# Kernel tuning notes

Hardware: AMD Instinct MI355X
Metric: run time of the kernel (lower is better)

## Reference

```python
import jax, jax.numpy as jnp
import numpy as np

H = 512

def _lstm_dir(seq, Wih, Whh, bih, bhh, reverse):
    # seq: [B,S,in]; Wih: [4H,in]; Whh: [4H,H]; biases [4H]
    B = seq.shape[0]
    xp = jnp.einsum('bsi,gi->bsg', seq, Wih) + bih  # precompute input projection [B,S,4H]
    h0 = jnp.zeros((B, H), seq.dtype)
    c0 = jnp.zeros((B, H), seq.dtype)

    def step(carry, xt):
        h, c = carry
        g = xt + h @ Whh.T + bhh
        i, f, gg, o = jnp.split(g, 4, axis=-1)
        c = jax.nn.sigmoid(f) * c + jax.nn.sigmoid(i) * jnp.tanh(gg)
        h = jax.nn.sigmoid(o) * jnp.tanh(c)
        return (h, c), h

    _, hs = jax.lax.scan(step, (h0, c0), jnp.swapaxes(xp, 0, 1), reverse=reverse)
    return jnp.swapaxes(hs, 0, 1)  # [B,S,H]


def setup_inputs() -> dict:
    key = jax.random.key(0)
    ks = jax.random.split(key, 24)
    B, S, E, V, C = 32, 512, 512, 32000, 2
    sc = 0.1
    d = {
        'x': jax.random.randint(ks[0], (B, S), 0, V, dtype=jnp.int32),
        'attention_mask': jnp.ones((B, S), dtype=jnp.int32),
        'emb': jax.random.normal(ks[1], (V, E), jnp.float32) * sc,
        'fc_W': jax.random.normal(ks[2], (C, 2 * H), jnp.float32) * sc,
        'fc_b': jax.random.normal(ks[3], (C,), jnp.float32) * sc,
    }
    i = 4
    for l, insz in [(0, E), (1, 2 * H)]:
        for dname in ('fwd', 'bwd'):
            d[f'{dname}_Wih{l}'] = jax.random.normal(ks[i], (4 * H, insz), jnp.float32) * sc; i += 1
            d[f'{dname}_Whh{l}'] = jax.random.normal(ks[i], (4 * H, H), jnp.float32) * sc; i += 1
            d[f'{dname}_bih{l}'] = jax.random.normal(ks[i], (4 * H,), jnp.float32) * sc; i += 1
            d[f'{dname}_bhh{l}'] = jax.random.normal(ks[i], (4 * H,), jnp.float32) * sc; i += 1
    return d


def reference(x, attention_mask, emb, fc_W, fc_b,
              fwd_Wih0, fwd_Whh0, fwd_bih0, fwd_bhh0,
              bwd_Wih0, bwd_Whh0, bwd_bih0, bwd_bhh0,
              fwd_Wih1, fwd_Whh1, fwd_bih1, fwd_bhh1,
              bwd_Wih1, bwd_Whh1, bwd_bih1, bwd_bhh1):
    out = emb[x]  # [B,S,E]
    layers = [
        ((fwd_Wih0, fwd_Whh0, fwd_bih0, fwd_bhh0), (bwd_Wih0, bwd_Whh0, bwd_bih0, bwd_bhh0)),
        ((fwd_Wih1, fwd_Whh1, fwd_bih1, fwd_bhh1), (bwd_Wih1, bwd_Whh1, bwd_bih1, bwd_bhh1)),
    ]
    for fw, bw in layers:
        f = _lstm_dir(out, *fw, reverse=False)
        b = _lstm_dir(out, *bw, reverse=True)
        out = jnp.concatenate([f, b], axis=-1)  # [B,S,2H]
        # dropout is identity in eval mode
    mask = attention_mask.astype(out.dtype)
    pooled = (out * mask[..., None]).sum(axis=1) / jnp.clip(mask.sum(axis=1, keepdims=True), 1e-9)
    logits = pooled @ fc_W.T + fc_b
    return logits
```

## Files before the change

kernel.cpp:

```cpp
#include <hip/hip_runtime.h>

typedef unsigned short u16;
typedef unsigned int   u32;
typedef unsigned long long u64;
typedef __attribute__((ext_vector_type(8))) short bf16x8;
typedef __attribute__((ext_vector_type(4))) float f32x4;

__device__ __forceinline__ u16 f2bf(float f) {
    u32 u; __builtin_memcpy(&u, &f, 4);
    u32 r = (u + 0x7FFFu + ((u >> 16) & 1u)) >> 16;
    return (u16)r;
}
__device__ __forceinline__ float bf2f(u16 h) {
    u32 u = ((u32)h) << 16; float f; __builtin_memcpy(&f, &u, 4); return f;
}
__device__ __forceinline__ float sigmoidf(float x) { return 1.f / (1.f + __expf(-x)); }
__device__ __forceinline__ float tanh_safe(float x) {
    float e = __expf(-2.f * fabsf(x));
    float t = (1.f - e) / (1.f + e);
    return x >= 0.f ? t : -t;
}

__global__ __launch_bounds__(256) void castk2(const float* __restrict__ s, u16* __restrict__ hi,
                                              u16* __restrict__ lo, int n) {
    int i = blockIdx.x * 256 + threadIdx.x;
    if (i < n) {
        float f = s[i];
        u16 h = f2bf(f);
        hi[i] = h;
        lo[i] = f2bf(f - bf2f(h));
    }
}

__global__ __launch_bounds__(256) void embed_cast(const int* __restrict__ x, const float* __restrict__ emb,
                                                  u16* __restrict__ x0) {
    int m = blockIdx.x;
    int idx = x[m];
    const float2* src = (const float2*)(emb + (size_t)idx * 512);
    u16* dst = x0 + (size_t)m * 512;
    int t = threadIdx.x;
    float2 v = src[t];
    dst[t * 2]     = f2bf(v.x);
    dst[t * 2 + 1] = f2bf(v.y);
}

__global__ __launch_bounds__(256) void gemm_bt(const u16* __restrict__ A, const u16* __restrict__ Bhi,
                                               const u16* __restrict__ Blo,
                                               u16* __restrict__ C, int M, int N, int K) {
    __shared__ __align__(16) u16 sA[128 * 32];
    __shared__ __align__(16) u16 sBh[128 * 32];
    __shared__ __align__(16) u16 sBl[128 * 32];
    const int tid  = threadIdx.x;
    const int lane = tid & 63, wave = tid >> 6;
    const int m0 = blockIdx.y * 128, n0 = blockIdx.x * 128;
    const int wm = (wave >> 1) * 64, wn = (wave & 1) * 64;
    f32x4 acc[4][4] = {};

    const int r0 = tid >> 2, c8 = (tid & 3) * 8;
    const int r1 = r0 + 64;
    const u16* Ap   = A   + (size_t)(m0 + r0) * K + c8;
    const u16* Ap2  = A   + (size_t)(m0 + r1) * K + c8;
    const u16* Bhp  = Bhi + (size_t)(n0 + r0) * K + c8;
    const u16* Bhp2 = Bhi + (size_t)(n0 + r1) * K + c8;
    const u16* Blp  = Blo + (size_t)(n0 + r0) * K + c8;
    const u16* Blp2 = Blo + (size_t)(n0 + r1) * K + c8;

    uint4 ra0, ra1, rh0, rh1, rl0, rl1;
    ra0 = *(const uint4*)(Ap);   ra1 = *(const uint4*)(Ap2);
    rh0 = *(const uint4*)(Bhp);  rh1 = *(const uint4*)(Bhp2);
    rl0 = *(const uint4*)(Blp);  rl1 = *(const uint4*)(Blp2);

    for (int kk = 0; kk < K; kk += 32) {
        __syncthreads();
        *(uint4*)(sA  + tid * 8)        = ra0;
        *(uint4*)(sA  + 2048 + tid * 8) = ra1;
        *(uint4*)(sBh + tid * 8)        = rh0;
        *(uint4*)(sBh + 2048 + tid * 8) = rh1;
        *(uint4*)(sBl + tid * 8)        = rl0;
        *(uint4*)(sBl + 2048 + tid * 8) = rl1;
        int kn = kk + 32;
        if (kn < K) {
            ra0 = *(const uint4*)(Ap + kn);   ra1 = *(const uint4*)(Ap2 + kn);
            rh0 = *(const uint4*)(Bhp + kn);  rh1 = *(const uint4*)(Bhp2 + kn);
            rl0 = *(const uint4*)(Blp + kn);  rl1 = *(const uint4*)(Blp2 + kn);
        }
        __syncthreads();
        bf16x8 av[4], bh[4], bl[4];
#pragma unroll
        for (int i = 0; i < 4; ++i) {
            av[i] = *(const bf16x8*)(sA  + (wm + i * 16 + (lane & 15)) * 32 + (lane >> 4) * 8);
            bh[i] = *(const bf16x8*)(sBh + (wn + i * 16 + (lane & 15)) * 32 + (lane >> 4) * 8);
            bl[i] = *(const bf16x8*)(sBl + (wn + i * 16 + (lane & 15)) * 32 + (lane >> 4) * 8);
        }
#pragma unroll
        for (int i = 0; i < 4; ++i)
#pragma unroll
            for (int j = 0; j < 4; ++j) {
                acc[i][j] = __builtin_amdgcn_mfma_f32_16x16x32_bf16(av[i], bh[j], acc[i][j], 0, 0, 0);
                acc[i][j] = __builtin_amdgcn_mfma_f32_16x16x32_bf16(av[i], bl[j], acc[i][j], 0, 0, 0);
            }
    }
#pragma unroll
    for (int i = 0; i < 4; ++i) {
        int m = m0 + wm + i * 16 + ((lane >> 4) << 2);
#pragma unroll
        for (int j = 0; j < 4; ++j) {
            int n = n0 + wn + j * 16 + (lane & 15);
#pragma unroll
            for (int rr = 0; rr < 4; ++rr)
                C[(size_t)(m + rr) * N + n] = f2bf(acc[i][j][rr]);
        }
    }
}

template <int LAYER>
__global__ __launch_bounds__(256, 1) void lstm_rec(
    const u16* __restrict__ xp_f, const u16* __restrict__ xp_b,
    const u16* __restrict__ whh_f_hi, const u16* __restrict__ whh_f_lo,
    const u16* __restrict__ whh_b_hi, const u16* __restrict__ whh_b_lo,
    const float* __restrict__ bih_f, const float* __restrict__ bhh_f,
    const float* __restrict__ bih_b, const float* __restrict__ bhh_b,
    u16* __restrict__ out0, float* __restrict__ pooled, const int* __restrict__ mask,
    u16* hbuf, u32* cnt)
{
    const int HP = 520;
    __shared__ __align__(16) u16  sHhi[32 * 520];
    __shared__ __align__(16) u16  sHlo[32 * 520];
    __shared__ __align__(16) u16  sXp[32 * 32];
    __shared__ __align__(16) float sG[32 * 33];
    __shared__ __align__(16) u16  sHoutHi[32 * 8];
    __shared__ __align__(16) u16  sHoutLo[32 * 8];

    const int tid = threadIdx.x;
    const int dir = blockIdx.x >> 6;
    const int slice = blockIdx.x & 63;
    const u16* xp     = dir ? xp_b : xp_f;
    const u16* whhH   = dir ? whh_b_hi : whh_f_hi;
    const u16* whhL   = dir ? whh_b_lo : whh_f_lo;
    const float* bih  = dir ? bih_b : bih_f;
    const float* bhh  = dir ? bhh_b : bhh_f;
    u16* hbD = hbuf + dir * 65536;
    u32* myCnt = cnt + dir * 64;

    const int wave = tid >> 6, lane = tid & 63;
    const int wm = (wave >> 1) * 16;
    const int wn = (wave & 1) * 16;
    bf16x8 wfragH[16], wfragL[16];
    {
        int n = wn + (lane & 15);
        int q = n >> 3, rr = n & 7;
        size_t rowoff = (size_t)(q * 512 + slice * 8 + rr) * 512 + (lane >> 4) * 8;
        const u16* wrh = whhH + rowoff;
        const u16* wrl = whhL + rowoff;
#pragma unroll
        for (int k2 = 0; k2 < 16; ++k2) {
            wfragH[k2] = *(const bf16x8*)(wrh + k2 * 32);
            wfragL[k2] = *(const bf16x8*)(wrl + k2 * 32);
        }
    }
    const int b = tid >> 3, r = tid & 7;
    float bias[4];
#pragma unroll
    for (int q = 0; q < 4; ++q) {
        int g = q * 512 + slice * 8 + r;
        bias[q] = bih[g] + bhh[g];
    }
    float cstate = 0.f, pool = 0.f;
    const int aoff = (wm + (lane & 15)) * HP + (lane >> 4) * 8;
    const int gRow = wm + ((lane >> 4) << 2), gCol = wn + (lane & 15);
    const int srow = tid >> 3, sc = tid & 7;

    for (int t = 0; t < 512; ++t) {
        const int tt = dir ? (511 - t) : t;
        if (tid < 128) {
            int xb = tid >> 2, xq = tid & 3;
            const uint4 v = *(const uint4*)(xp + ((size_t)(xb * 512 + tt)) * 2048 + xq * 512 + slice * 8);
            *(uint4*)(sXp + xb * 32 + xq * 8) = v;
        }
        if (t > 0) {
            if (tid == 0) {
                u32 tgt = 64u * (u32)t;
                while (__hip_atomic_load(myCnt, __ATOMIC_RELAXED, __HIP_MEMORY_SCOPE_AGENT) < tgt)
                    __builtin_amdgcn_s_sleep(1);
            }
            __syncthreads();
            {
                const u16* hp = hbD + ((t - 1) & 1) * 32768 + srow * 512;
                const u16* lp = hp + 16384;
                u16* dhi = sHhi + srow * HP;
                u16* dlo = sHlo + srow * HP;
#pragma unroll
                for (int j = 0; j < 8; ++j) {
                    int ch = sc + 8 * j;
                    u64 a0 = __hip_atomic_load((const u64*)(hp + ch * 8),     __ATOMIC_RELAXED, __HIP_MEMORY_SCOPE_AGENT);
                    u64 a1 = __hip_atomic_load((const u64*)(hp + ch * 8) + 1, __ATOMIC_RELAXED, __HIP_MEMORY_SCOPE_AGENT);
                    u64 b0 = __hip_atomic_load((const u64*)(lp + ch * 8),     __ATOMIC_RELAXED, __HIP_MEMORY_SCOPE_AGENT);
                    u64 b1 = __hip_atomic_load((const u64*)(lp + ch * 8) + 1, __ATOMIC_RELAXED, __HIP_MEMORY_SCOPE_AGENT);
                    *(u64*)(dhi + ch * 8)     = a0;
                    *(u64*)(dhi + ch * 8 + 4) = a1;
                    *(u64*)(dlo + ch * 8)     = b0;
                    *(u64*)(dlo + ch * 8 + 4) = b1;
                }
            }
        }
        __syncthreads();
        f32x4 acc = {};
        if (t > 0) {
#pragma unroll
            for (int k2 = 0; k2 < 16; ++k2) {
                bf16x8 ah = *(const bf16x8*)(sHhi + aoff + k2 * 32);
                bf16x8 al = *(const bf16x8*)(sHlo + aoff + k2 * 32);
                acc = __builtin_amdgcn_mfma_f32_16x16x32_bf16(ah, wfragH[k2], acc, 0, 0, 0);
                acc = __builtin_amdgcn_mfma_f32_16x16x32_bf16(al, wfragH[k2], acc, 0, 0, 0);
                acc = __builtin_amdgcn_mfma_f32_16x16x32_bf16(ah, wfragL[k2], acc, 0, 0, 0);
            }
        }
#pragma unroll
        for (int rr = 0; rr < 4; ++rr) sG[(gRow + rr) * 33 + gCol] = acc[rr];
        __syncthreads();
        {
            float gq[4];
#pragma unroll
            for (int q = 0; q < 4; ++q)
                gq[q] = sG[b * 33 + q * 8 + r] + bf2f(sXp[b * 32 + q * 8 + r]) + bias[q];
            float ig = sigmoidf(gq[0]), fg = sigmoidf(gq[1]);
            float gg = tanh_safe(gq[2]), og = sigmoidf(gq[3]);
            cstate = fg * cstate + ig * gg;
            float h = og * tanh_safe(cstate);
            u16 hh = f2bf(h);
            if (LAYER == 0) {
                out0[((size_t)(b * 512 + tt)) * 1024 + dir * 512 + slice * 8 + r] = hh;
            } else {
                pool += h * (float)mask[b * 512 + tt];
            }
            sHoutHi[b * 8 + r] = hh;
            sHoutLo[b * 8 + r] = f2bf(h - bf2f(hh));
        }
        __syncthreads();
        if (tid < 128) {
            int w = tid;
            int pb = w >> 2, d = w & 3;
            u32 vh = ((const u32*)sHoutHi)[w];
            u32 vl = ((const u32*)sHoutLo)[w];
            u32* gh = (u32*)(hbD + (t & 1) * 32768 + pb * 512 + slice * 8) + d;
            u32* gl = (u32*)(hbD + (t & 1) * 32768 + 16384 + pb * 512 + slice * 8) + d;
            __hip_atomic_store(gh, vh, __ATOMIC_RELAXED, __HIP_MEMORY_SCOPE_AGENT);
            __hip_atomic_store(gl, vl, __ATOMIC_RELAXED, __HIP_MEMORY_SCOPE_AGENT);
        }
        __syncthreads();
        if (tid == 0)
            __hip_atomic_fetch_add(myCnt, 1u, __ATOMIC_RELEASE, __HIP_MEMORY_SCOPE_AGENT);
    }
    if (LAYER == 1)
        pooled[(size_t)b * 1024 + dir * 512 + slice * 8 + r] = pool;
}

__global__ __launch_bounds__(256) void final_fc(const float* __restrict__ pooled, const int* __restrict__ mask,
                                                const float* __restrict__ fcW, const float* __restrict__ fcb,
                                                float* __restrict__ out) {
    __shared__ float red[256];
    int tid = threadIdx.x;
    int pair = tid & 63, kc = tid >> 6;
    int b = pair >> 1, c = pair & 1;
    float s = 0.f;
    for (int k = kc * 256; k < kc * 256 + 256; ++k)
        s += pooled[b * 1024 + k] * fcW[c * 1024 + k];
    red[tid] = s;
    __syncthreads();
    if (kc == 0) {
        float tot = red[pair] + red[64 + pair] + red[128 + pair] + red[192 + pair];
        float ms = 0.f;
        for (int t = 0; t < 512; ++t) ms += (float)mask[b * 512 + t];
        ms = fmaxf(ms, 1e-9f);
        out[b * 2 + c] = tot / ms + fcb[c];
    }
}

extern "C" void kernel_launch(void* const* d_in, const int* in_sizes, int n_in,
                              void* d_out, int out_size, void* d_ws, size_t ws_size,
                              hipStream_t stream) {
    (void)in_sizes; (void)n_in; (void)out_size; (void)ws_size;
    const int*   x     = (const int*)d_in[0];
    const int*   amask = (const int*)d_in[1];
    const float* emb   = (const float*)d_in[2];
    const float* fcW   = (const float*)d_in[3];
    const float* fcb   = (const float*)d_in[4];
    const float* fWih0 = (const float*)d_in[5];
    const float* fWhh0 = (const float*)d_in[6];
    const float* fbih0 = (const float*)d_in[7];
    const float* fbhh0 = (const float*)d_in[8];
    const float* bWih0 = (const float*)d_in[9];
    const float* bWhh0 = (const float*)d_in[10];
    const float* bbih0 = (const float*)d_in[11];
    const float* bbhh0 = (const float*)d_in[12];
    const float* fWih1 = (const float*)d_in[13];
    const float* fWhh1 = (const float*)d_in[14];
    const float* fbih1 = (const float*)d_in[15];
    const float* fbhh1 = (const float*)d_in[16];
    const float* bWih1 = (const float*)d_in[17];
    const float* bWhh1 = (const float*)d_in[18];
    const float* bbih1 = (const float*)d_in[19];
    const float* bbhh1 = (const float*)d_in[20];

    char* ws = (char*)d_ws;
    size_t off = 0;
    auto alloc = [&](size_t bytes) { void* p = ws + off; off += (bytes + 1023) & ~(size_t)1023; return p; };
    u16* x0    = (u16*)alloc((size_t)16384 * 512 * 2);
    u16* xpf   = (u16*)alloc((size_t)16384 * 2048 * 2);
    u16* xpb   = (u16*)alloc((size_t)16384 * 2048 * 2);
    u16* out0  = (u16*)alloc((size_t)16384 * 1024 * 2);
    u16* wih0fH = (u16*)alloc((size_t)2048 * 512 * 2);
    u16* wih0fL = (u16*)alloc((size_t)2048 * 512 * 2);
    u16* wih0bH = (u16*)alloc((size_t)2048 * 512 * 2);
    u16* wih0bL = (u16*)alloc((size_t)2048 * 512 * 2);
    u16* whh0fH = (u16*)alloc((size_t)2048 * 512 * 2);
    u16* whh0fL = (u16*)alloc((size_t)2048 * 512 * 2);
    u16* whh0bH = (u16*)alloc((size_t)2048 * 512 * 2);
    u16* whh0bL = (u16*)alloc((size_t)2048 * 512 * 2);
    u16* wih1fH = (u16*)alloc((size_t)2048 * 1024 * 2);
    u16* wih1fL = (u16*)alloc((size_t)2048 * 1024 * 2);
    u16* wih1bH = (u16*)alloc((size_t)2048 * 1024 * 2);
    u16* wih1bL = (u16*)alloc((size_t)2048 * 1024 * 2);
    u16* whh1fH = (u16*)alloc((size_t)2048 * 512 * 2);
    u16* whh1fL = (u16*)alloc((size_t)2048 * 512 * 2);
    u16* whh1bH = (u16*)alloc((size_t)2048 * 512 * 2);
    u16* whh1bL = (u16*)alloc((size_t)2048 * 512 * 2);
    float* pooled = (float*)alloc((size_t)32 * 1024 * 4);
    u16* hbuf  = (u16*)alloc((size_t)2 * 2 * 2 * 32 * 512 * 2);
    u32* cnt   = (u32*)alloc(1024);

    hipMemsetAsync(cnt, 0, 1024, stream);

    const int NW0 = 2048 * 512, NW1 = 2048 * 1024;
    castk2<<<dim3((NW0 + 255) / 256), 256, 0, stream>>>(fWih0, wih0fH, wih0fL, NW0);
    castk2<<<dim3((NW0 + 255) / 256), 256, 0, stream>>>(bWih0, wih0bH, wih0bL, NW0);
    castk2<<<dim3((NW0 + 255) / 256), 256, 0, stream>>>(fWhh0, whh0fH, whh0fL, NW0);
    castk2<<<dim3((NW0 + 255) / 256), 256, 0, stream>>>(bWhh0, whh0bH, whh0bL, NW0);
    castk2<<<dim3((NW1 + 255) / 256), 256, 0, stream>>>(fWih1, wih1fH, wih1fL, NW1);
    castk2<<<dim3((NW1 + 255) / 256), 256, 0, stream>>>(bWih1, wih1bH, wih1bL, NW1);
    castk2<<<dim3((NW0 + 255) / 256), 256, 0, stream>>>(fWhh1, whh1fH, whh1fL, NW0);
    castk2<<<dim3((NW0 + 255) / 256), 256, 0, stream>>>(bWhh1, whh1bH, whh1bL, NW0);

    embed_cast<<<dim3(16384), 256, 0, stream>>>(x, emb, x0);

    gemm_bt<<<dim3(16, 128), 256, 0, stream>>>(x0, wih0fH, wih0fL, xpf, 16384, 2048, 512);
    gemm_bt<<<dim3(16, 128), 256, 0, stream>>>(x0, wih0bH, wih0bL, xpb, 16384, 2048, 512);
    lstm_rec<0><<<dim3(128), 256, 0, stream>>>(xpf, xpb, whh0fH, whh0fL, whh0bH, whh0bL,
                                               fbih0, fbhh0, bbih0, bbhh0,
                                               out0, nullptr, nullptr, hbuf, cnt);
    gemm_bt<<<dim3(16, 128), 256, 0, stream>>>(out0, wih1fH, wih1fL, xpf, 16384, 2048, 1024);
    gemm_bt<<<dim3(16, 128), 256, 0, stream>>>(out0, wih1bH, wih1bL, xpb, 16384, 2048, 1024);
    lstm_rec<1><<<dim3(128), 256, 0, stream>>>(xpf, xpb, whh1fH, whh1fL, whh1bH, whh1bL,
                                               fbih1, fbhh1, bbih1, bbhh1,
                                               nullptr, pooled, amask, hbuf, cnt + 128);

    final_fc<<<dim3(1), 256, 0, stream>>>(pooled, amask, fcW, fcb, (float*)d_out);
}
```

Before: 7.697 ms.

## Replace shared counter with per-block step flags and move low weights to LDS

The single atomic counter that every block incremented each timestep is replaced by one flag per block, spaced 16 bytes apart. Each block stores its step number with release semantics, and 64 lanes of the waiting block poll all flags together using a wave-wide all-vote. The low-precision half of the recurrent weights moves from registers into shared memory to cut register pressure. The hidden-state exchange now uses wider, batched loads and 64-bit stores. This is meant to cut atomic contention and per-step latency on the serial recurrence, at the cost of more polling traffic and extra LDS reads in the MFMA loop.

```diff
diff --git a/kernel.cpp b/kernel.cpp
--- a/kernel.cpp
+++ b/kernel.cpp
@@ -121,11 +121,12 @@
     const float* __restrict__ bih_f, const float* __restrict__ bhh_f,
     const float* __restrict__ bih_b, const float* __restrict__ bhh_b,
     u16* __restrict__ out0, float* __restrict__ pooled, const int* __restrict__ mask,
-    u16* hbuf, u32* cnt)
+    u16* hbuf, u32* flags)
 {
     const int HP = 520;
     __shared__ __align__(16) u16  sHhi[32 * 520];
     __shared__ __align__(16) u16  sHlo[32 * 520];
+    __shared__ __align__(16) u16  sWlo[32 * 520];
     __shared__ __align__(16) u16  sXp[32 * 32];
     __shared__ __align__(16) float sG[32 * 33];
     __shared__ __align__(16) u16  sHoutHi[32 * 8];
@@ -140,24 +141,32 @@
     const float* bih  = dir ? bih_b : bih_f;
     const float* bhh  = dir ? bhh_b : bhh_f;
     u16* hbD = hbuf + dir * 65536;
-    u32* myCnt = cnt + dir * 64;
+    u32* myFlags = flags + dir * 256;
 
     const int wave = tid >> 6, lane = tid & 63;
     const int wm = (wave >> 1) * 16;
     const int wn = (wave & 1) * 16;
-    bf16x8 wfragH[16], wfragL[16];
+
+    bf16x8 wfragH[16];
     {
         int n = wn + (lane & 15);
         int q = n >> 3, rr = n & 7;
-        size_t rowoff = (size_t)(q * 512 + slice * 8 + rr) * 512 + (lane >> 4) * 8;
-        const u16* wrh = whhH + rowoff;
-        const u16* wrl = whhL + rowoff;
-#pragma unroll
-        for (int k2 = 0; k2 < 16; ++k2) {
-            wfragH[k2] = *(const bf16x8*)(wrh + k2 * 32);
-            wfragL[k2] = *(const bf16x8*)(wrl + k2 * 32);
-        }
-    }
+        const u16* wrh = whhH + (size_t)(q * 512 + slice * 8 + rr) * 512 + (lane >> 4) * 8;
+#pragma unroll
+        for (int k2 = 0; k2 < 16; ++k2) wfragH[k2] = *(const bf16x8*)(wrh + k2 * 32);
+    }
+    {
+        int c = tid >> 3;
+        int grow = (c >> 3) * 512 + slice * 8 + (c & 7);
+        const u16* src = whhL + (size_t)grow * 512;
+        u16* dst = sWlo + c * HP;
+#pragma unroll
+        for (int jj = 0; jj < 8; ++jj) {
+            int ch = (tid & 7) + 8 * jj;
+            *(uint4*)(dst + ch * 8) = *(const uint4*)(src + ch * 8);
+        }
+    }
+
     const int b = tid >> 3, r = tid & 7;
     float bias[4];
 #pragma unroll
@@ -167,8 +176,10 @@
     }
     float cstate = 0.f, pool = 0.f;
     const int aoff = (wm + (lane & 15)) * HP + (lane >> 4) * 8;
+    const int boff = (wn + (lane & 15)) * HP + (lane >> 4) * 8;
     const int gRow = wm + ((lane >> 4) << 2), gCol = wn + (lane & 15);
     const int srow = tid >> 3, sc = tid & 7;
+    __syncthreads();
 
     for (int t = 0; t < 512; ++t) {
         const int tt = dir ? (511 - t) : t;
@@ -178,28 +189,33 @@
             *(uint4*)(sXp + xb * 32 + xq * 8) = v;
         }
         if (t > 0) {
-            if (tid == 0) {
-                u32 tgt = 64u * (u32)t;
-                while (__hip_atomic_load(myCnt, __ATOMIC_RELAXED, __HIP_MEMORY_SCOPE_AGENT) < tgt)
+            if (tid < 64) {
+                const u32* fp = myFlags + tid * 4;
+                for (;;) {
+                    u32 v = __hip_atomic_load(fp, __ATOMIC_ACQUIRE, __HIP_MEMORY_SCOPE_AGENT);
+                    if (__all((int)(v >= (u32)t))) break;
                     __builtin_amdgcn_s_sleep(1);
+                }
             }
             __syncthreads();
             {
-                const u16* hp = hbD + ((t - 1) & 1) * 32768 + srow * 512;
+                const u16* hp = hbD + ((t - 1) & 1) * 32768 + srow * 512 + sc * 64;
                 const u16* lp = hp + 16384;
-                u16* dhi = sHhi + srow * HP;
-                u16* dlo = sHlo + srow * HP;
+                u64 rh[16], rl[16];
+#pragma unroll
+                for (int j = 0; j < 16; ++j)
+                    rh[j] = __hip_atomic_load((const u64*)hp + j, __ATOMIC_RELAXED, __HIP_MEMORY_SCOPE_AGENT);
+#pragma unroll
+                for (int j = 0; j < 16; ++j)
+                    rl[j] = __hip_atomic_load((const u64*)lp + j, __ATOMIC_RELAXED, __HIP_MEMORY_SCOPE_AGENT);
+                u16* dhi = sHhi + srow * HP + sc * 64;
+                u16* dlo = sHlo + srow * HP + sc * 64;
 #pragma unroll
                 for (int j = 0; j < 8; ++j) {
-                    int ch = sc + 8 * j;
-                    u64 a0 = __hip_atomic_load((const u64*)(hp + ch * 8),     __ATOMIC_RELAXED, __HIP_MEMORY_SCOPE_AGENT);
-                    u64 a1 = __hip_atomic_load((const u64*)(hp + ch * 8) + 1, __ATOMIC_RELAXED, __HIP_MEMORY_SCOPE_AGENT);
-                    u64 b0 = __hip_atomic_load((const u64*)(lp + ch * 8),     __ATOMIC_RELAXED, __HIP_MEMORY_SCOPE_AGENT);
-                    u64 b1 = __hip_atomic_load((const u64*)(lp + ch * 8) + 1, __ATOMIC_RELAXED, __HIP_MEMORY_SCOPE_AGENT);
-                    *(u64*)(dhi + ch * 8)     = a0;
-                    *(u64*)(dhi + ch * 8 + 4) = a1;
-                    *(u64*)(dlo + ch * 8)     = b0;
-                    *(u64*)(dlo + ch * 8 + 4) = b1;
+                    uint4 vh; __builtin_memcpy(&vh, &rh[j * 2], 16);
+                    uint4 vl; __builtin_memcpy(&vl, &rl[j * 2], 16);
+                    *(uint4*)(dhi + j * 8) = vh;
+                    *(uint4*)(dlo + j * 8) = vl;
                 }
             }
         }
@@ -210,9 +226,10 @@
             for (int k2 = 0; k2 < 16; ++k2) {
                 bf16x8 ah = *(const bf16x8*)(sHhi + aoff + k2 * 32);
                 bf16x8 al = *(const bf16x8*)(sHlo + aoff + k2 * 32);
+                bf16x8 bl = *(const bf16x8*)(sWlo + boff + k2 * 32);
                 acc = __builtin_amdgcn_mfma_f32_16x16x32_bf16(ah, wfragH[k2], acc, 0, 0, 0);
                 acc = __builtin_amdgcn_mfma_f32_16x16x32_bf16(al, wfragH[k2], acc, 0, 0, 0);
-                acc = __builtin_amdgcn_mfma_f32_16x16x32_bf16(ah, wfragL[k2], acc, 0, 0, 0);
+                acc = __builtin_amdgcn_mfma_f32_16x16x32_bf16(ah, bl,         acc, 0, 0, 0);
             }
         }
 #pragma unroll
@@ -238,18 +255,15 @@
         }
         __syncthreads();
         if (tid < 128) {
-            int w = tid;
-            int pb = w >> 2, d = w & 3;
-            u32 vh = ((const u32*)sHoutHi)[w];
-            u32 vl = ((const u32*)sHoutLo)[w];
-            u32* gh = (u32*)(hbD + (t & 1) * 32768 + pb * 512 + slice * 8) + d;
-            u32* gl = (u32*)(hbD + (t & 1) * 32768 + 16384 + pb * 512 + slice * 8) + d;
-            __hip_atomic_store(gh, vh, __ATOMIC_RELAXED, __HIP_MEMORY_SCOPE_AGENT);
-            __hip_atomic_store(gl, vl, __ATOMIC_RELAXED, __HIP_MEMORY_SCOPE_AGENT);
+            int plane = tid >> 6;
+            int w = tid & 63, row = w >> 1, half = w & 1;
+            u64 v = plane ? ((const u64*)sHoutLo)[w] : ((const u64*)sHoutHi)[w];
+            u64* g = (u64*)(hbD + (t & 1) * 32768 + plane * 16384 + row * 512 + slice * 8) + half;
+            __hip_atomic_store(g, v, __ATOMIC_RELAXED, __HIP_MEMORY_SCOPE_AGENT);
         }
         __syncthreads();
         if (tid == 0)
-            __hip_atomic_fetch_add(myCnt, 1u, __ATOMIC_RELEASE, __HIP_MEMORY_SCOPE_AGENT);
+            __hip_atomic_store(myFlags + slice * 4, (u32)(t + 1), __ATOMIC_RELEASE, __HIP_MEMORY_SCOPE_AGENT);
     }
     if (LAYER == 1)
         pooled[(size_t)b * 1024 + dir * 512 + slice * 8 + r] = pool;
@@ -327,9 +341,9 @@
     u16* whh1bL = (u16*)alloc((size_t)2048 * 512 * 2);
     float* pooled = (float*)alloc((size_t)32 * 1024 * 4);
     u16* hbuf  = (u16*)alloc((size_t)2 * 2 * 2 * 32 * 512 * 2);
-    u32* cnt   = (u32*)alloc(1024);
-
-    hipMemsetAsync(cnt, 0, 1024, stream);
+    u32* flg   = (u32*)alloc(8192);
+
+    hipMemsetAsync(flg, 0, 8192, stream);
 
     const int NW0 = 2048 * 512, NW1 = 2048 * 1024;
     castk2<<<dim3((NW0 + 255) / 256), 256, 0, stream>>>(fWih0, wih0fH, wih0fL, NW0);
@@ -347,12 +361,12 @@
     gemm_bt<<<dim3(16, 128), 256, 0, stream>>>(x0, wih0bH, wih0bL, xpb, 16384, 2048, 512);
     lstm_rec<0><<<dim3(128), 256, 0, stream>>>(xpf, xpb, whh0fH, whh0fL, whh0bH, whh0bL,
                                                fbih0, fbhh0, bbih0, bbhh0,
-                                               out0, nullptr, nullptr, hbuf, cnt);
+                                               out0, nullptr, nullptr, hbuf, flg);
     gemm_bt<<<dim3(16, 128), 256, 0, stream>>>(out0, wih1fH, wih1fL, xpf, 16384, 2048, 1024);
     gemm_bt<<<dim3(16, 128), 256, 0, stream>>>(out0, wih1bH, wih1bL, xpb, 16384, 2048, 1024);
     lstm_rec<1><<<dim3(128), 256, 0, stream>>>(xpf, xpb, whh1fH, whh1fL, whh1bH, whh1bL,
                                                fbih1, fbhh1, bbih1, bbhh1,
-                                               nullptr, pooled, amask, hbuf, cnt + 128);
+                                               nullptr, pooled, amask, hbuf, flg + 1024);
 
     final_fc<<<dim3(1), 256, 0, stream>>>(pooled, amask, fcW, fcb, (float*)d_out);
 }
```

After: 11.87 ms. +54.3%, slower.
